# Performance work log

Hardware: AMD Instinct MI355X
Metric: run time of the kernel (lower is better)

Reference implementation:

```python
import jax, jax.numpy as jnp
import numpy as np

B, L, D, N, R = 8, 4096, 768, 16, 8

def setup_inputs() -> dict:
    key = jax.random.key(0)
    ks = jax.random.split(key, 12)
    return {
        "x": jax.random.normal(ks[0], (B, L, D), jnp.float32),
        "a_logit": jnp.zeros((N,), jnp.float32),
        "U": jax.random.normal(ks[1], (N, R), jnp.float32) * 0.02,
        "V": jax.random.normal(ks[2], (N, R), jnp.float32) * 0.02,
        "W_in": jax.random.normal(ks[3], (N, D), jnp.float32) * (1.0 / np.sqrt(D)),
        "b_in": jax.random.normal(ks[4], (N,), jnp.float32) * 0.02,
        "W_gate": jax.random.normal(ks[5], (N, D), jnp.float32) * (1.0 / np.sqrt(D)),
        "b_gate": jax.random.normal(ks[6], (N,), jnp.float32) * 0.02,
        "W_out": jax.random.normal(ks[7], (D, N), jnp.float32) * (1.0 / np.sqrt(N)),
        "b_out": jax.random.normal(ks[8], (D,), jnp.float32) * 0.02,
        "W_skip": jax.random.normal(ks[9], (D, D), jnp.float32) * (1.0 / np.sqrt(D)),
        "b_skip": jax.random.normal(ks[10], (D,), jnp.float32) * 0.02,
    }

def reference(x, a_logit, U, V, W_in, b_in, W_gate, b_gate, W_out, b_out, W_skip, b_skip):
    # x: [B, L, D]
    u = jnp.einsum('bld,nd->bln', x, W_in) + b_in            # [B, L, N]
    g = jax.nn.sigmoid(jnp.einsum('bld,nd->bln', x, W_gate) + b_gate)
    a = jax.nn.sigmoid(a_logit)                              # [N]
    lowrank_T = V @ U.T                                      # (U @ V.T).T, [N, N]
    gu = g * u                                               # [B, L, N]

    def step(h, gu_t):
        # h: [B, N]; h_new = a*h + g_t*u_t + h @ lowrank.T
        h = h * a + gu_t + h @ lowrank_T
        return h, h

    h0 = jnp.zeros((x.shape[0], a_logit.shape[0]), x.dtype)
    _, hs = jax.lax.scan(step, h0, jnp.swapaxes(gu, 0, 1))   # hs: [L, B, N]
    hs = jnp.swapaxes(hs, 0, 1)                              # [B, L, N]
    # batched out_proj + skip across all timesteps
    y = jnp.einsum('bln,dn->bld', hs, W_out) + b_out \
        + jnp.einsum('ble,de->bld', x, W_skip) + b_skip
    return y
```

## Files before the change

### kernel.cpp

```cpp
#include <hip/hip_runtime.h>
#include <hip/hip_bf16.h>
#include <math.h>

#define BB 8
#define LL 4096
#define DD 768
#define NN 16
#define RR 8
#define MROWS (BB*LL)
#define KAUG 800
#define CCH 64
#define NCH (LL/CCH)

typedef unsigned int u32;
typedef unsigned short u16;
typedef __attribute__((ext_vector_type(8))) short short8;
typedef __attribute__((ext_vector_type(4))) float f32x4;
typedef __attribute__((ext_vector_type(4))) unsigned short us4;
typedef __attribute__((ext_vector_type(4))) u32 u32x4;

__device__ __forceinline__ u16 f2bf(float f) {
  u32 u = __float_as_uint(f);
  u32 r = (u + 0x7fffu + ((u >> 16) & 1u)) >> 16;
  return (u16)r;
}

__device__ __forceinline__ u32 pk2bf(float a, float b) {
  __hip_bfloat162 h = __float22bfloat162_rn(make_float2(a, b));
  return *reinterpret_cast<u32*>(&h);
}

__device__ __forceinline__ void gload_lds16(const void* g, void* l) {
  __builtin_amdgcn_global_load_lds(
      (const __attribute__((address_space(1))) u32*)g,
      (__attribute__((address_space(3))) u32*)l, 16, 0, 0);
}

__global__ void k_prep(const float* __restrict__ a_logit, const float* __restrict__ U,
                       const float* __restrict__ V, const float* __restrict__ b_out,
                       const float* __restrict__ b_skip,
                       float* __restrict__ Mw, float* __restrict__ MCw,
                       float* __restrict__ bsum) {
  __shared__ float cur[256];
  __shared__ float nxt[256];
  int t = threadIdx.x;
  int m = t >> 4, n = t & 15;
  float s = 0.f;
  #pragma unroll
  for (int r = 0; r < RR; r++) s += V[m*RR+r] * U[n*RR+r];
  if (m == n) s += 1.f / (1.f + expf(-a_logit[n]));
  cur[t] = s;
  Mw[t] = s;
  __syncthreads();
  for (int it = 0; it < 6; ++it) {
    float acc = 0.f;
    #pragma unroll
    for (int k = 0; k < 16; k++) acc += cur[m*16+k] * cur[k*16+n];
    nxt[t] = acc;
    __syncthreads();
    cur[t] = nxt[t];
    __syncthreads();
  }
  MCw[t] = cur[t];
  for (int d = t; d < DD; d += 256) bsum[d] = b_out[d] + b_skip[d];
}

__global__ void k_weights(const float* __restrict__ W_skip, const float* __restrict__ W_out,
                          const float* __restrict__ W_in, const float* __restrict__ W_gate,
                          u16* __restrict__ Waug, u16* __restrict__ WinG) {
  int bid = blockIdx.x;
  int t = threadIdx.x;
  if (bid < DD) {
    int d = bid;
    for (int c = t; c < KAUG; c += 256) {
      float v;
      if (c < DD)           v = W_skip[d*DD + c];
      else if (c < DD+NN)   v = W_out[d*NN + (c-DD)];
      else                  v = 0.f;
      Waug[d*KAUG + c] = f2bf(v);
    }
  } else {
    int r = bid - DD;
    const float* Wsrc = (r < NN) ? (W_in + r*DD) : (W_gate + (r-NN)*DD);
    for (int c = t; c < DD; c += 256) WinG[r*DD + c] = f2bf(Wsrc[c]);
  }
}

__global__ __launch_bounds__(256) void k_gu(const float* __restrict__ x,
                                            const u16* __restrict__ WinG,
                                            const float* __restrict__ b_in,
                                            const float* __restrict__ b_gate,
                                            float* __restrict__ gu_T) {
  __shared__ u16 At[128*32];
  __shared__ u16 Bt[32*32];
  int tid = threadIdx.x;
  int wave = tid >> 6, lane = tid & 63;
  int rowbase = blockIdx.x * 128;
  int r = tid >> 1, ch = tid & 1;
  const float* xrow = x + (long)(rowbase + r)*DD + ch*16;
  f32x4 acc[2][2] = {};
  for (int it = 0; it < DD/32; ++it) {
    int k0 = it * 32;
    {
      const float4* xp = (const float4*)(xrow + k0);
      float4 f0 = xp[0], f1 = xp[1], f2 = xp[2], f3 = xp[3];
      u32x4 lo, hi;
      lo.x = pk2bf(f0.x,f0.y); lo.y = pk2bf(f0.z,f0.w);
      lo.z = pk2bf(f1.x,f1.y); lo.w = pk2bf(f1.z,f1.w);
      hi.x = pk2bf(f2.x,f2.y); hi.y = pk2bf(f2.z,f2.w);
      hi.z = pk2bf(f3.x,f3.y); hi.w = pk2bf(f3.z,f3.w);
      *(u32x4*)(At + r*32 + ch*16)     = lo;
      *(u32x4*)(At + r*32 + ch*16 + 8) = hi;
    }
    if (tid < 128) {
      int br = tid >> 2, co = tid & 3;
      gload_lds16(WinG + br*DD + k0 + co*8, Bt + tid*8);
    }
    __syncthreads();
    int l15 = lane & 15, lh = lane >> 4;
    short8 a[2], b[2];
    #pragma unroll
    for (int i = 0; i < 2; i++)
      a[i] = *(const short8*)(At + (wave*32 + i*16 + l15)*32 + lh*8);
    #pragma unroll
    for (int j = 0; j < 2; j++)
      b[j] = *(const short8*)(Bt + (j*16 + l15)*32 + lh*8);
    #pragma unroll
    for (int i = 0; i < 2; i++)
      #pragma unroll
      for (int j = 0; j < 2; j++)
        acc[i][j] = __builtin_amdgcn_mfma_f32_16x16x32_bf16(a[i], b[j], acc[i][j], 0, 0, 0);
    __syncthreads();
  }
  int l15 = lane & 15, lh = lane >> 4;
  float bi = b_in[l15], bg = b_gate[l15];
  #pragma unroll
  for (int i = 0; i < 2; i++) {
    int row0 = rowbase + wave*32 + i*16 + lh*4;
    int b = row0 >> 12;
    int t0 = row0 & 4095;
    float4 o;
    {
      float u0 = acc[i][0][0] + bi, u1 = acc[i][0][1] + bi;
      float u2 = acc[i][0][2] + bi, u3 = acc[i][0][3] + bi;
      float g0 = 1.f/(1.f+__expf(-(acc[i][1][0]+bg)));
      float g1 = 1.f/(1.f+__expf(-(acc[i][1][1]+bg)));
      float g2 = 1.f/(1.f+__expf(-(acc[i][1][2]+bg)));
      float g3 = 1.f/(1.f+__expf(-(acc[i][1][3]+bg)));
      o.x = g0*u0; o.y = g1*u1; o.z = g2*u2; o.w = g3*u3;
    }
    *(float4*)(gu_T + ((long)(b*16 + l15) << 12) + t0) = o;
  }
}

__global__ void k_scan_local(const float* __restrict__ gu_T, const float* __restrict__ Mw,
                             float* __restrict__ cend) {
  int lane = threadIdx.x & 63;
  int grp = lane >> 4, n = lane & 15;
  int cid = blockIdx.x*4 + grp;
  int b = cid >> 6, k = cid & 63;
  float Mcol[16];
  #pragma unroll
  for (int m = 0; m < 16; m++) Mcol[m] = Mw[m*16 + n];
  const float4* g4 = (const float4*)(gu_T + ((long)(b*16 + n) << 12) + k*CCH);
  float gv[CCH];
  #pragma unroll
  for (int q = 0; q < CCH/4; q++) {
    float4 v = g4[q];
    gv[q*4+0]=v.x; gv[q*4+1]=v.y; gv[q*4+2]=v.z; gv[q*4+3]=v.w;
  }
  float h = 0.f;
  #pragma unroll
  for (int t = 0; t < CCH; t++) {
    float hn = gv[t];
    #pragma unroll
    for (int m = 0; m < 16; m++) hn += __shfl(h, m, 16) * Mcol[m];
    h = hn;
  }
  cend[(b*NCH + k)*NN + n] = h;
}

__global__ void k_scan_prefix(const float* __restrict__ cend, const float* __restrict__ MCw,
                              float* __restrict__ Hstart) {
  __shared__ float s[BB*NCH*NN];
  int t = threadIdx.x;
  for (int i = t; i < BB*NCH*NN; i += 256) s[i] = cend[i];
  __syncthreads();
  if (t < 128) {
    int b = t >> 4, n = t & 15;
    float Mcol[16];
    #pragma unroll
    for (int m = 0; m < 16; m++) Mcol[m] = MCw[m*16 + n];
    float h = 0.f;
    for (int k = 0; k < NCH; k++) {
      Hstart[(b*NCH + k)*NN + n] = h;
      float hn = s[(b*NCH + k)*NN + n];
      #pragma unroll
      for (int m = 0; m < 16; m++) hn += __shfl(h, m, 16) * Mcol[m];
      h = hn;
    }
  }
}

__global__ void k_scan_final(const float* __restrict__ gu_T, const float* __restrict__ Mw,
                             const float* __restrict__ Hstart, u16* __restrict__ hs) {
  int lane = threadIdx.x & 63;
  int grp = lane >> 4, n = lane & 15;
  int cid = blockIdx.x*4 + grp;
  int b = cid >> 6, k = cid & 63;
  float Mcol[16];
  #pragma unroll
  for (int m = 0; m < 16; m++) Mcol[m] = Mw[m*16 + n];
  const float4* g4 = (const float4*)(gu_T + ((long)(b*16 + n) << 12) + k*CCH);
  float gv[CCH];
  #pragma unroll
  for (int q = 0; q < CCH/4; q++) {
    float4 v = g4[q];
    gv[q*4+0]=v.x; gv[q*4+1]=v.y; gv[q*4+2]=v.z; gv[q*4+3]=v.w;
  }
  float h = Hstart[(b*NCH + k)*NN + n];
  u16* hp = hs + ((long)(b*LL) + k*CCH)*NN + n;
  #pragma unroll
  for (int t = 0; t < CCH; t++) {
    float hn = gv[t];
    #pragma unroll
    for (int m = 0; m < 16; m++) hn += __shfl(h, m, 16) * Mcol[m];
    h = hn;
    hp[(long)t*NN] = f2bf(h);
  }
}

__global__ __launch_bounds__(256) void k_out(const float* __restrict__ x,
                                             const u16* __restrict__ hs,
                                             const u16* __restrict__ Waug,
                                             const float* __restrict__ bsum,
                                             float* __restrict__ y) {
  __shared__ u16 At[128*32];
  __shared__ u16 Bt[128*32];
  int tid = threadIdx.x;
  int wave = tid >> 6, lane = tid & 63;
  int wm = wave >> 1, wn = wave & 1;
  int rowbase = blockIdx.x * 128;
  int colbase = blockIdx.y * 128;
  int r = tid >> 1, ch = tid & 1;
  const float* xrow = x + (long)(rowbase + r)*DD + ch*16;
  f32x4 acc[4][4] = {};
  for (int it = 0; it < 25; ++it) {
    int k0 = it * 32;
    #pragma unroll
    for (int p = 0; p < 2; p++) {
      int cc = tid + p*256;
      int br = cc >> 2, bco = cc & 3;
      gload_lds16(Waug + (long)(colbase + br)*KAUG + k0 + bco*8, Bt + cc*8);
    }
    if (it < 24) {
      const float4* xp = (const float4*)(xrow + k0);
      float4 f0 = xp[0], f1 = xp[1], f2 = xp[2], f3 = xp[3];
      u32x4 lo, hi;
      lo.x = pk2bf(f0.x,f0.y); lo.y = pk2bf(f0.z,f0.w);
      lo.z = pk2bf(f1.x,f1.y); lo.w = pk2bf(f1.z,f1.w);
      hi.x = pk2bf(f2.x,f2.y); hi.y = pk2bf(f2.z,f2.w);
      hi.z = pk2bf(f3.x,f3.y); hi.w = pk2bf(f3.z,f3.w);
      *(u32x4*)(At + r*32 + ch*16)     = lo;
      *(u32x4*)(At + r*32 + ch*16 + 8) = hi;
    } else {
      if (ch == 0) {
        const u32x4* hp = (const u32x4*)(hs + (long)(rowbase + r)*NN);
        *(u32x4*)(At + r*32)     = hp[0];
        *(u32x4*)(At + r*32 + 8) = hp[1];
      } else {
        u32x4 z = (u32x4)0;
        *(u32x4*)(At + r*32 + 16) = z;
        *(u32x4*)(At + r*32 + 24) = z;
      }
    }
    __syncthreads();
    int l15 = lane & 15, lh = lane >> 4;
    short8 a[4], b[4];
    #pragma unroll
    for (int i = 0; i < 4; i++)
      a[i] = *(const short8*)(At + (wm*64 + i*16 + l15)*32 + lh*8);
    #pragma unroll
    for (int j = 0; j < 4; j++)
      b[j] = *(const short8*)(Bt + (wn*64 + j*16 + l15)*32 + lh*8);
    #pragma unroll
    for (int i = 0; i < 4; i++)
      #pragma unroll
      for (int j = 0; j < 4; j++)
        acc[i][j] = __builtin_amdgcn_mfma_f32_16x16x32_bf16(a[i], b[j], acc[i][j], 0, 0, 0);
    __syncthreads();
  }
  int l15 = lane & 15, lh = lane >> 4;
  #pragma unroll
  for (int j = 0; j < 4; j++) {
    int col = colbase + wn*64 + j*16 + l15;
    float bs = bsum[col];
    #pragma unroll
    for (int i = 0; i < 4; i++) {
      int row0 = rowbase + wm*64 + i*16 + lh*4;
      #pragma unroll
      for (int rr = 0; rr < 4; rr++)
        y[(long)(row0 + rr)*DD + col] = acc[i][j][rr] + bs;
    }
  }
}

extern "C" void kernel_launch(void* const* d_in, const int* in_sizes, int n_in,
                              void* d_out, int out_size, void* d_ws, size_t ws_size,
                              hipStream_t stream) {
  (void)in_sizes; (void)n_in; (void)out_size; (void)ws_size;
  const float* x       = (const float*)d_in[0];
  const float* a_logit = (const float*)d_in[1];
  const float* U       = (const float*)d_in[2];
  const float* V       = (const float*)d_in[3];
  const float* W_in    = (const float*)d_in[4];
  const float* b_in    = (const float*)d_in[5];
  const float* W_gate  = (const float*)d_in[6];
  const float* b_gate  = (const float*)d_in[7];
  const float* W_out   = (const float*)d_in[8];
  const float* b_out   = (const float*)d_in[9];
  const float* W_skip  = (const float*)d_in[10];
  const float* b_skip  = (const float*)d_in[11];

  char* ws = (char*)d_ws;
  u16*   Waug = (u16*)(ws + 0);
  u16*   WinG = (u16*)(ws + 1228800);
  float* gu_T = (float*)(ws + 1277952);
  u16*   hs   = (u16*)(ws + 3375104);
  float* Mw   = (float*)(ws + 4423680);
  float* MCw  = (float*)(ws + 4424704);
  float* cend = (float*)(ws + 4425728);
  float* Hst  = (float*)(ws + 4458496);
  float* bsum = (float*)(ws + 4491264);
  float* y    = (float*)d_out;

  hipLaunchKernelGGL(k_prep,        dim3(1),      dim3(256), 0, stream,
                     a_logit, U, V, b_out, b_skip, Mw, MCw, bsum);
  hipLaunchKernelGGL(k_weights,     dim3(800),    dim3(256), 0, stream,
                     W_skip, W_out, W_in, W_gate, Waug, WinG);
  hipLaunchKernelGGL(k_gu,          dim3(256),    dim3(256), 0, stream,
                     x, WinG, b_in, b_gate, gu_T);
  hipLaunchKernelGGL(k_scan_local,  dim3(128),    dim3(64),  0, stream, gu_T, Mw, cend);
  hipLaunchKernelGGL(k_scan_prefix, dim3(1),      dim3(256), 0, stream, cend, MCw, Hst);
  hipLaunchKernelGGL(k_scan_final,  dim3(128),    dim3(64),  0, stream, gu_T, Mw, Hst, hs);
  hipLaunchKernelGGL(k_out,         dim3(256, 6), dim3(256), 0, stream,
                     x, hs, Waug, bsum, y);
}
```

Baseline: 330.4 us.

## Materialize bf16 augmented activations and fuse three scan kernels into one

```diff
diff --git a/kernel.cpp b/kernel.cpp
--- a/kernel.cpp
+++ b/kernel.cpp
@@ -16,7 +16,6 @@
 typedef unsigned short u16;
 typedef __attribute__((ext_vector_type(8))) short short8;
 typedef __attribute__((ext_vector_type(4))) float f32x4;
-typedef __attribute__((ext_vector_type(4))) unsigned short us4;
 typedef __attribute__((ext_vector_type(4))) u32 u32x4;
 
 __device__ __forceinline__ u16 f2bf(float f) {
@@ -90,7 +89,8 @@
                                             const u16* __restrict__ WinG,
                                             const float* __restrict__ b_in,
                                             const float* __restrict__ b_gate,
-                                            float* __restrict__ gu_T) {
+                                            float* __restrict__ gu_T,
+                                            u16* __restrict__ Xaug) {
   __shared__ u16 At[128*32];
   __shared__ u16 Bt[32*32];
   int tid = threadIdx.x;
@@ -98,6 +98,7 @@
   int rowbase = blockIdx.x * 128;
   int r = tid >> 1, ch = tid & 1;
   const float* xrow = x + (long)(rowbase + r)*DD + ch*16;
+  u16* xarow = Xaug + (long)(rowbase + r)*KAUG + ch*16;
   f32x4 acc[2][2] = {};
   for (int it = 0; it < DD/32; ++it) {
     int k0 = it * 32;
@@ -111,6 +112,8 @@
       hi.z = pk2bf(f3.x,f3.y); hi.w = pk2bf(f3.z,f3.w);
       *(u32x4*)(At + r*32 + ch*16)     = lo;
       *(u32x4*)(At + r*32 + ch*16 + 8) = hi;
+      *(u32x4*)(xarow + k0)     = lo;
+      *(u32x4*)(xarow + k0 + 8) = hi;
     }
     if (tid < 128) {
       int br = tid >> 2, co = tid & 3;
@@ -132,6 +135,7 @@
         acc[i][j] = __builtin_amdgcn_mfma_f32_16x16x32_bf16(a[i], b[j], acc[i][j], 0, 0, 0);
     __syncthreads();
   }
+  *(u32x4*)(Xaug + (long)(rowbase + r)*KAUG + 784 + ch*8) = (u32x4)0;
   int l15 = lane & 15, lh = lane >> 4;
   float bi = b_in[l15], bg = b_gate[l15];
   #pragma unroll
@@ -153,16 +157,19 @@
   }
 }
 
-__global__ void k_scan_local(const float* __restrict__ gu_T, const float* __restrict__ Mw,
-                             float* __restrict__ cend) {
-  int lane = threadIdx.x & 63;
-  int grp = lane >> 4, n = lane & 15;
-  int cid = blockIdx.x*4 + grp;
-  int b = cid >> 6, k = cid & 63;
+__global__ __launch_bounds__(1024, 4) void k_scan(const float* __restrict__ gu_T,
+                                                  const float* __restrict__ Mw,
+                                                  const float* __restrict__ MCw,
+                                                  u16* __restrict__ Xaug) {
+  __shared__ float cend_s[NCH*NN];
+  __shared__ float hst_s[NCH*NN];
+  int b = blockIdx.x;
+  int tid = threadIdx.x;
+  int c = tid >> 4, n = tid & 15;
   float Mcol[16];
   #pragma unroll
   for (int m = 0; m < 16; m++) Mcol[m] = Mw[m*16 + n];
-  const float4* g4 = (const float4*)(gu_T + ((long)(b*16 + n) << 12) + k*CCH);
+  const float4* g4 = (const float4*)(gu_T + ((long)(b*16 + n) << 12) + c*CCH);
   float gv[CCH];
   #pragma unroll
   for (int q = 0; q < CCH/4; q++) {
@@ -177,102 +184,54 @@
     for (int m = 0; m < 16; m++) hn += __shfl(h, m, 16) * Mcol[m];
     h = hn;
   }
-  cend[(b*NCH + k)*NN + n] = h;
-}
-
-__global__ void k_scan_prefix(const float* __restrict__ cend, const float* __restrict__ MCw,
-                              float* __restrict__ Hstart) {
-  __shared__ float s[BB*NCH*NN];
-  int t = threadIdx.x;
-  for (int i = t; i < BB*NCH*NN; i += 256) s[i] = cend[i];
+  cend_s[c*16 + n] = h;
   __syncthreads();
-  if (t < 128) {
-    int b = t >> 4, n = t & 15;
-    float Mcol[16];
-    #pragma unroll
-    for (int m = 0; m < 16; m++) Mcol[m] = MCw[m*16 + n];
-    float h = 0.f;
+  if (tid < 16) {
+    float MCcol[16];
+    #pragma unroll
+    for (int m = 0; m < 16; m++) MCcol[m] = MCw[m*16 + tid];
+    float hp = 0.f;
     for (int k = 0; k < NCH; k++) {
-      Hstart[(b*NCH + k)*NN + n] = h;
-      float hn = s[(b*NCH + k)*NN + n];
+      hst_s[k*16 + tid] = hp;
+      float hn = cend_s[k*16 + tid];
       #pragma unroll
-      for (int m = 0; m < 16; m++) hn += __shfl(h, m, 16) * Mcol[m];
-      h = hn;
-    }
-  }
-}
-
-__global__ void k_scan_final(const float* __restrict__ gu_T, const float* __restrict__ Mw,
-                             const float* __restrict__ Hstart, u16* __restrict__ hs) {
-  int lane = threadIdx.x & 63;
-  int grp = lane >> 4, n = lane & 15;
-  int cid = blockIdx.x*4 + grp;
-  int b = cid >> 6, k = cid & 63;
-  float Mcol[16];
-  #pragma unroll
-  for (int m = 0; m < 16; m++) Mcol[m] = Mw[m*16 + n];
-  const float4* g4 = (const float4*)(gu_T + ((long)(b*16 + n) << 12) + k*CCH);
-  float gv[CCH];
-  #pragma unroll
-  for (int q = 0; q < CCH/4; q++) {
-    float4 v = g4[q];
-    gv[q*4+0]=v.x; gv[q*4+1]=v.y; gv[q*4+2]=v.z; gv[q*4+3]=v.w;
-  }
-  float h = Hstart[(b*NCH + k)*NN + n];
-  u16* hp = hs + ((long)(b*LL) + k*CCH)*NN + n;
+      for (int m = 0; m < 16; m++) hn += __shfl(hp, m, 16) * MCcol[m];
+      hp = hn;
+    }
+  }
+  __syncthreads();
+  float h2 = hst_s[c*16 + n];
+  u16* xa = Xaug + ((long)(b*LL) + c*CCH)*KAUG + DD + n;
   #pragma unroll
   for (int t = 0; t < CCH; t++) {
     float hn = gv[t];
     #pragma unroll
-    for (int m = 0; m < 16; m++) hn += __shfl(h, m, 16) * Mcol[m];
-    h = hn;
-    hp[(long)t*NN] = f2bf(h);
-  }
-}
-
-__global__ __launch_bounds__(256) void k_out(const float* __restrict__ x,
-                                             const u16* __restrict__ hs,
+    for (int m = 0; m < 16; m++) hn += __shfl(h2, m, 16) * Mcol[m];
+    h2 = hn;
+    xa[(long)t*KAUG] = f2bf(h2);
+  }
+}
+
+__global__ __launch_bounds__(256) void k_out(const u16* __restrict__ Xaug,
                                              const u16* __restrict__ Waug,
                                              const float* __restrict__ bsum,
-                                             float* __restrict__ y) {
+                                             float* __restrict__ y, int colofs) {
   __shared__ u16 At[128*32];
   __shared__ u16 Bt[128*32];
   int tid = threadIdx.x;
   int wave = tid >> 6, lane = tid & 63;
   int wm = wave >> 1, wn = wave & 1;
   int rowbase = blockIdx.x * 128;
-  int colbase = blockIdx.y * 128;
-  int r = tid >> 1, ch = tid & 1;
-  const float* xrow = x + (long)(rowbase + r)*DD + ch*16;
+  int colbase = (blockIdx.y + colofs) * 128;
   f32x4 acc[4][4] = {};
-  for (int it = 0; it < 25; ++it) {
+  for (int it = 0; it < KAUG/32; ++it) {
     int k0 = it * 32;
     #pragma unroll
     for (int p = 0; p < 2; p++) {
       int cc = tid + p*256;
-      int br = cc >> 2, bco = cc & 3;
-      gload_lds16(Waug + (long)(colbase + br)*KAUG + k0 + bco*8, Bt + cc*8);
-    }
-    if (it < 24) {
-      const float4* xp = (const float4*)(xrow + k0);
-      float4 f0 = xp[0], f1 = xp[1], f2 = xp[2], f3 = xp[3];
-      u32x4 lo, hi;
-      lo.x = pk2bf(f0.x,f0.y); lo.y = pk2bf(f0.z,f0.w);
-      lo.z = pk2bf(f1.x,f1.y); lo.w = pk2bf(f1.z,f1.w);
-      hi.x = pk2bf(f2.x,f2.y); hi.y = pk2bf(f2.z,f2.w);
-      hi.z = pk2bf(f3.x,f3.y); hi.w = pk2bf(f3.z,f3.w);
-      *(u32x4*)(At + r*32 + ch*16)     = lo;
-      *(u32x4*)(At + r*32 + ch*16 + 8) = hi;
-    } else {
-      if (ch == 0) {
-        const u32x4* hp = (const u32x4*)(hs + (long)(rowbase + r)*NN);
-        *(u32x4*)(At + r*32)     = hp[0];
-        *(u32x4*)(At + r*32 + 8) = hp[1];
-      } else {
-        u32x4 z = (u32x4)0;
-        *(u32x4*)(At + r*32 + 16) = z;
-        *(u32x4*)(At + r*32 + 24) = z;
-      }
+      int r = cc >> 2, co = cc & 3;
+      gload_lds16(Xaug + (long)(rowbase + r)*KAUG + k0 + co*8, At + cc*8);
+      gload_lds16(Waug + (long)(colbase + r)*KAUG + k0 + co*8, Bt + cc*8);
     }
     __syncthreads();
     int l15 = lane & 15, lh = lane >> 4;
@@ -323,26 +282,25 @@
   const float* b_skip  = (const float*)d_in[11];
 
   char* ws = (char*)d_ws;
-  u16*   Waug = (u16*)(ws + 0);
-  u16*   WinG = (u16*)(ws + 1228800);
-  float* gu_T = (float*)(ws + 1277952);
-  u16*   hs   = (u16*)(ws + 3375104);
-  float* Mw   = (float*)(ws + 4423680);
-  float* MCw  = (float*)(ws + 4424704);
-  float* cend = (float*)(ws + 4425728);
-  float* Hst  = (float*)(ws + 4458496);
-  float* bsum = (float*)(ws + 4491264);
+  u16*   Xaug = (u16*)(ws + 0);
+  u16*   Waug = (u16*)(ws + 52428800);
+  u16*   WinG = (u16*)(ws + 53657600);
+  float* gu_T = (float*)(ws + 53706752);
+  float* Mw   = (float*)(ws + 55803904);
+  float* MCw  = (float*)(ws + 55804928);
+  float* bsum = (float*)(ws + 55805952);
   float* y    = (float*)d_out;
 
-  hipLaunchKernelGGL(k_prep,        dim3(1),      dim3(256), 0, stream,
+  hipLaunchKernelGGL(k_prep,    dim3(1),      dim3(256),  0, stream,
                      a_logit, U, V, b_out, b_skip, Mw, MCw, bsum);
-  hipLaunchKernelGGL(k_weights,     dim3(800),    dim3(256), 0, stream,
+  hipLaunchKernelGGL(k_weights, dim3(800),    dim3(256),  0, stream,
                      W_skip, W_out, W_in, W_gate, Waug, WinG);
-  hipLaunchKernelGGL(k_gu,          dim3(256),    dim3(256), 0, stream,
-                     x, WinG, b_in, b_gate, gu_T);
-  hipLaunchKernelGGL(k_scan_local,  dim3(128),    dim3(64),  0, stream, gu_T, Mw, cend);
-  hipLaunchKernelGGL(k_scan_prefix, dim3(1),      dim3(256), 0, stream, cend, MCw, Hst);
-  hipLaunchKernelGGL(k_scan_final,  dim3(128),    dim3(64),  0, stream, gu_T, Mw, Hst, hs);
-  hipLaunchKernelGGL(k_out,         dim3(256, 6), dim3(256), 0, stream,
-                     x, hs, Waug, bsum, y);
-}
+  hipLaunchKernelGGL(k_gu,      dim3(256),    dim3(256),  0, stream,
+                     x, WinG, b_in, b_gate, gu_T, Xaug);
+  hipLaunchKernelGGL(k_scan,    dim3(BB),     dim3(1024), 0, stream,
+                     gu_T, Mw, MCw, Xaug);
+  hipLaunchKernelGGL(k_out,     dim3(256, 3), dim3(256),  0, stream,
+                     Xaug, Waug, bsum, y, 0);
+  hipLaunchKernelGGL(k_out,     dim3(256, 3), dim3(256),  0, stream,
+                     Xaug, Waug, bsum, y, 3);
+}
```

Result: slower. 403.5 us (+22.1%).
